# Optimization experiments

Measured on AMD Instinct MI355X. Metric: run time of the kernel, lower is better.

The kernel has to match this reference:

```python
import jax, jax.numpy as jnp
import numpy as np

N_NODES = 200000
N_FRAGS = 50000
N_EDGES = 400000
HDIM = 128
VOCAB = 800


def setup_inputs() -> dict:
    key = jax.random.key(0)
    ks = jax.random.split(key, 9)
    x = jax.random.normal(ks[0], (N_NODES, HDIM), dtype=jnp.float32)
    fragments = jax.random.uniform(ks[1], (N_FRAGS, VOCAB), dtype=jnp.float32)
    emb_table = jax.random.normal(ks[2], (VOCAB, HDIM), dtype=jnp.float32)
    W_f = jax.random.normal(ks[3], (HDIM, HDIM), dtype=jnp.float32) / np.sqrt(HDIM)
    b_f = jax.random.normal(ks[4], (HDIM,), dtype=jnp.float32) * 0.01
    W_s = jax.random.normal(ks[5], (2 * HDIM, HDIM), dtype=jnp.float32) / np.sqrt(2 * HDIM)
    b_s = jax.random.normal(ks[6], (HDIM,), dtype=jnp.float32) * 0.01
    row = jax.random.randint(ks[7], (N_EDGES,), 0, N_NODES, dtype=jnp.int32)
    col = jax.random.randint(ks[8], (N_EDGES,), 0, N_FRAGS, dtype=jnp.int32)
    return {"x": x, "fragments": fragments, "emb_table": emb_table,
            "W_f": W_f, "b_f": b_f, "W_s": W_s, "b_s": b_s,
            "row": row, "col": col}


def _scatter_mean(vals, idx, num_segments):
    s = jax.ops.segment_sum(vals, idx, num_segments=num_segments)
    cnt = jax.ops.segment_sum(jnp.ones((vals.shape[0], 1), vals.dtype), idx,
                              num_segments=num_segments)
    return s / jnp.maximum(cnt, 1.0)


def reference(x, fragments, emb_table, W_f, b_f, W_s, b_s, row, col):
    N, H = x.shape
    F = fragments.shape[0]
    # gather node feats along memberships, mean-pool per fragment: [F, H]
    substructure_x = _scatter_mean(x[row], col, F)
    # fragment type embedding branch
    frag_ids = jnp.argmax(fragments, axis=1)            # [F]
    fragments_emb = emb_table[frag_ids] @ W_f + b_f      # [F, H]
    substructure_x = jnp.concatenate([substructure_x, fragments_emb], axis=1)  # [F, 2H]
    fragment_emb = substructure_x @ W_s + b_s            # [F, H]
    # gather fragment embeddings back to memberships, mean-pool per node: [N, H]
    return _scatter_mean(fragment_emb[col], row, N)
```

## Files before the change

### kernel.cpp

```cpp
#include <hip/hip_runtime.h>

#define HDIM 128
#define VOCAB 800
#define FB 32
#define NB 64
#define TILE 1024
#define TILE_N 512

typedef float f4 __attribute__((ext_vector_type(4)));
typedef float f2 __attribute__((ext_vector_type(2)));

#define ACC8(pa, pb, h) { \
    pa.x += __uint_as_float(h.x << 16); \
    pa.y += __uint_as_float(h.x & 0xffff0000u); \
    pa.z += __uint_as_float(h.y << 16); \
    pa.w += __uint_as_float(h.y & 0xffff0000u); \
    pb.x += __uint_as_float(h.z << 16); \
    pb.y += __uint_as_float(h.z & 0xffff0000u); \
    pb.z += __uint_as_float(h.w << 16); \
    pb.w += __uint_as_float(h.w & 0xffff0000u); }

static __device__ __forceinline__ unsigned short f2bf(float f) {
    unsigned int u = __float_as_uint(f);
    return (unsigned short)((u + 0x7fffu + ((u >> 16) & 1u)) >> 16);
}

__global__ void k_amc(const float* __restrict__ frags, int* __restrict__ frag_id,
                      const float* __restrict__ x, unsigned short* __restrict__ xb,
                      const int* __restrict__ row, const int* __restrict__ col,
                      int* __restrict__ cnt,
                      const float* __restrict__ emb, const float* __restrict__ W_f,
                      const float* __restrict__ W_s, const float* __restrict__ b_f,
                      const float* __restrict__ b_s, float* __restrict__ E2,
                      float* __restrict__ bfs, int F) {
    __shared__ float e[2][HDIM], t1[2][HDIM];
    int b = blockIdx.x, t = threadIdx.x;
    if (b < 12500) {
        int wave = b * 4 + (t >> 6);
        int lane = t & 63;
        const f4* r = reinterpret_cast<const f4*>(frags + (size_t)wave * VOCAB);
        float best = -1e30f;
        int bidx = 0;
        for (int i = lane; i < VOCAB / 4; i += 64) {
            f4 v = __builtin_nontemporal_load(r + i);
            int base = i * 4;
            if (v.x > best) { best = v.x; bidx = base + 0; }
            if (v.y > best) { best = v.y; bidx = base + 1; }
            if (v.z > best) { best = v.z; bidx = base + 2; }
            if (v.w > best) { best = v.w; bidx = base + 3; }
        }
        for (int off = 32; off > 0; off >>= 1) {
            float ov = __shfl_xor(best, off, 64);
            int   oi = __shfl_xor(bidx, off, 64);
            if (ov > best || (ov == best && oi < bidx)) { best = ov; bidx = oi; }
        }
        if (lane == 0) frag_id[wave] = bidx;
    } else if (b < 12891) {
        int i = (b - 12500) * 256 + t;
        if (i < 100000) {
            int4 r4 = reinterpret_cast<const int4*>(row)[i];
            int4 c4 = reinterpret_cast<const int4*>(col)[i];
            atomicAdd(&cnt[F + r4.x], 1); atomicAdd(&cnt[F + r4.y], 1);
            atomicAdd(&cnt[F + r4.z], 1); atomicAdd(&cnt[F + r4.w], 1);
            atomicAdd(&cnt[c4.x], 1); atomicAdd(&cnt[c4.y], 1);
            atomicAdd(&cnt[c4.z], 1); atomicAdd(&cnt[c4.w], 1);
        }
    } else if (b < 25391) {
        size_t i = (size_t)(b - 12891) * 256 + t;
        const f4* xp = reinterpret_cast<const f4*>(x);
        f4 v0 = __builtin_nontemporal_load(xp + 2 * i);
        f4 v1 = __builtin_nontemporal_load(xp + 2 * i + 1);
        uint4 o;
        o.x = (unsigned)f2bf(v0.x) | ((unsigned)f2bf(v0.y) << 16);
        o.y = (unsigned)f2bf(v0.z) | ((unsigned)f2bf(v0.w) << 16);
        o.z = (unsigned)f2bf(v1.x) | ((unsigned)f2bf(v1.y) << 16);
        o.w = (unsigned)f2bf(v1.z) | ((unsigned)f2bf(v1.w) << 16);
        *reinterpret_cast<uint4*>(xb + i * 8) = o;
    } else {
        int bp = b - 25391;
        int j = t & 127, half = t >> 7;
        if (bp < 400) {
            int v = bp * 2 + half;
            e[half][j] = emb[(size_t)v * HDIM + j];
            __syncthreads();
            float a = 0.f;
            for (int k = 0; k < HDIM; ++k)
                a = fmaf(e[half][k], W_f[k * HDIM + j], a);
            t1[half][j] = a;
            __syncthreads();
            float bb = 0.f;
            for (int k = 0; k < HDIM; ++k)
                bb = fmaf(t1[half][k], W_s[(HDIM + k) * HDIM + j], bb);
            E2[(size_t)v * HDIM + j] = bb;
        } else {
            if (half == 0) e[0][j] = b_f[j];
            __syncthreads();
            if (half == 0) {
                float bb = b_s[j];
                for (int k = 0; k < HDIM; ++k)
                    bb = fmaf(e[0][k], W_s[(HDIM + k) * HDIM + j], bb);
                bfs[j] = bb;
            }
        }
    }
}

__global__ void k_bsum(const int* __restrict__ cnt, int L, int* __restrict__ bsum) {
    __shared__ int s[256];
    int t = threadIdx.x;
    int i = blockIdx.x * 256 + t;
    s[t] = (i < L) ? cnt[i] : 0;
    __syncthreads();
    for (int o = 128; o > 0; o >>= 1) {
        if (t < o) s[t] += s[t + o];
        __syncthreads();
    }
    if (t == 0) bsum[blockIdx.x] = s[0];
}

__global__ void k_scan(int* __restrict__ bsum, int nb) {
    __shared__ int s[1024];
    int t = threadIdx.x;
    int v = (t < nb) ? bsum[t] : 0;
    s[t] = v;
    __syncthreads();
    for (int o = 1; o < 1024; o <<= 1) {
        int a = (t >= o) ? s[t - o] : 0;
        __syncthreads();
        s[t] += a;
        __syncthreads();
    }
    if (t < nb) bsum[t] = s[t] - v;
}

__global__ void k_base(const int* __restrict__ cnt, const int* __restrict__ bsum, int L,
                       int* __restrict__ base) {
    __shared__ int s[256];
    int t = threadIdx.x;
    int i = blockIdx.x * 256 + t;
    int v = (i < L) ? cnt[i] : 0;
    s[t] = v;
    __syncthreads();
    for (int o = 1; o < 256; o <<= 1) {
        int a = (t >= o) ? s[t - o] : 0;
        __syncthreads();
        s[t] += a;
        __syncthreads();
    }
    if (i < L) base[i] = bsum[blockIdx.x] + s[t] - v;
}

__global__ void k_place(const int* __restrict__ row, const int* __restrict__ col,
                        int* __restrict__ base, int* __restrict__ pay, int F, int E) {
    int i = blockIdx.x * 256 + threadIdx.x;
    if (i >= E / 4) return;
    int4 r4 = reinterpret_cast<const int4*>(row)[i];
    int4 c4 = reinterpret_cast<const int4*>(col)[i];
#define PL(r, c) { \
    int pc = atomicAdd(&base[c], 1); pay[pc] = r; \
    int pr = atomicAdd(&base[F + r], 1); pay[pr] = c; }
    PL(r4.x, c4.x) PL(r4.y, c4.y) PL(r4.z, c4.z) PL(r4.w, c4.w)
#undef PL
}

__global__ __launch_bounds__(256) void k_frag(
        const unsigned short* __restrict__ xb, const int* __restrict__ base,
        const int* __restrict__ pay, const int* __restrict__ frag_id,
        const float* __restrict__ W_s, const float* __restrict__ E2,
        const float* __restrict__ bfs, unsigned short* __restrict__ fembb, int F, int E) {
    __shared__ f2 sI[FB / 2][HDIM];
    __shared__ int eidx[TILE];
    __shared__ int cb[FB + 1];
    int t = threadIdx.x;
    int sg = t >> 4, l = t & 15;
    int fb = blockIdx.x * FB;
    if (t <= FB) {
        int idx = fb + t - 1;
        cb[t] = (idx < 0) ? 0 : ((idx < F) ? base[idx] : E);
    }
    __syncthreads();
    int st0 = cb[sg],      d0 = cb[sg + 1] - st0;
    int st1 = cb[16 + sg], d1 = cb[17 + sg] - st1;
    int p0 = cb[0], pend = cb[FB];
    const uint4* x4 = reinterpret_cast<const uint4*>(xb);
    float4 z = make_float4(0.f, 0.f, 0.f, 0.f);
    float4 a0A0 = z, a0A1 = z, a0B0 = z, a0B1 = z;
    float4 a1A0 = z, a1A1 = z, a1B0 = z, a1B1 = z;
    for (int tb = p0; tb < pend; tb += TILE) {
        int nload = min(TILE, pend - tb);
        for (int i = t; i < nload; i += 256) eidx[i] = pay[tb + i];
        __syncthreads();
        int lim = tb + nload;
        int lo0 = max(st0, tb) - tb, hi0 = min(st0 + d0, lim) - tb;
        int lo1 = max(st1, tb) - tb, hi1 = min(st1 + d1, lim) - tb;
        int m = max(hi0 - lo0, hi1 - lo1);
        for (int j = 0; j < m; j += 2) {
            if (lo0 + j < hi0)     { uint4 h = x4[(size_t)eidx[lo0 + j]     * 16 + l]; ACC8(a0A0, a0A1, h); }
            if (lo0 + j + 1 < hi0) { uint4 h = x4[(size_t)eidx[lo0 + j + 1] * 16 + l]; ACC8(a0B0, a0B1, h); }
            if (lo1 + j < hi1)     { uint4 h = x4[(size_t)eidx[lo1 + j]     * 16 + l]; ACC8(a1A0, a1A1, h); }
            if (lo1 + j + 1 < hi1) { uint4 h = x4[(size_t)eidx[lo1 + j + 1] * 16 + l]; ACC8(a1B0, a1B1, h); }
        }
        __syncthreads();
    }
    {
        float inv0 = 1.0f / fmaxf((float)d0, 1.0f);
        float inv1 = 1.0f / fmaxf((float)d1, 1.0f);
        int pr0 = sg >> 1, pa0 = sg & 1;
        int pr1 = (16 + sg) >> 1, pa1 = sg & 1;
        float v0[8] = { (a0A0.x + a0B0.x) * inv0, (a0A0.y + a0B0.y) * inv0,
                        (a0A0.z + a0B0.z) * inv0, (a0A0.w + a0B0.w) * inv0,
                        (a0A1.x + a0B1.x) * inv0, (a0A1.y + a0B1.y) * inv0,
                        (a0A1.z + a0B1.z) * inv0, (a0A1.w + a0B1.w) * inv0 };
        float v1[8] = { (a1A0.x + a1B0.x) * inv1, (a1A0.y + a1B0.y) * inv1,
                        (a1A0.z + a1B0.z) * inv1, (a1A0.w + a1B0.w) * inv1,
                        (a1A1.x + a1B1.x) * inv1, (a1A1.y + a1B1.y) * inv1,
                        (a1A1.z + a1B1.z) * inv1, (a1A1.w + a1B1.w) * inv1 };
#pragma unroll
        for (int i = 0; i < 8; ++i) {
            ((float*)&sI[pr0][8 * l + i])[pa0] = v0[i];
            ((float*)&sI[pr1][8 * l + i])[pa1] = v1[i];
        }
    }
    __syncthreads();
    int d = t & 127;
    int fh = t >> 7;
    float bv = bfs[d];
    f2 acc2[8];
#pragma unroll
    for (int q = 0; q < 8; ++q) {
        int pr = fh * 8 + q;
        int fA = fb + 2 * pr, fB = fA + 1;
        int idA = frag_id[min(fA, F - 1)];
        int idB = frag_id[min(fB, F - 1)];
        acc2[q].x = E2[(size_t)idA * HDIM + d] + bv;
        acc2[q].y = E2[(size_t)idB * HDIM + d] + bv;
    }
    for (int k = 0; k < HDIM; k += 2) {
        float w0 = W_s[(k + 0) * HDIM + d];
        float w1 = W_s[(k + 1) * HDIM + d];
        f2 w0v; w0v.x = w0; w0v.y = w0;
        f2 w1v; w1v.x = w1; w1v.y = w1;
#pragma unroll
        for (int q = 0; q < 8; ++q) {
            int pr = fh * 8 + q;
            f2 vv0 = sI[pr][k];
            f2 vv1 = sI[pr][k + 1];
            acc2[q] += vv0 * w0v + vv1 * w1v;
        }
    }
#pragma unroll
    for (int q = 0; q < 8; ++q) {
        int pr = fh * 8 + q;
        int fA = fb + 2 * pr;
        if (fA < F)     fembb[(size_t)fA * HDIM + d]       = f2bf(acc2[q].x);
        if (fA + 1 < F) fembb[(size_t)(fA + 1) * HDIM + d] = f2bf(acc2[q].y);
    }
}

__global__ __launch_bounds__(256) void k_node(
        const unsigned short* __restrict__ fembb, const int* __restrict__ base,
        const int* __restrict__ pay, float* __restrict__ out, int F, int E, int N) {
    __shared__ int eidx[TILE_N];
    __shared__ int cb[NB + 1];
    int t = threadIdx.x;
    int sg = t >> 4, l = t & 15;
    int n0 = blockIdx.x * NB;
    if (t <= NB) {
        int idx = n0 + t - 1;
        cb[t] = (idx < 0) ? E : base[F + idx];
    }
    __syncthreads();
    int st_[4], dg_[4];
    float4 z = make_float4(0.f, 0.f, 0.f, 0.f);
    float4 aA0[4] = {z, z, z, z}, aA1[4] = {z, z, z, z};
    float4 aB0[4] = {z, z, z, z}, aB1[4] = {z, z, z, z};
#pragma unroll
    for (int q = 0; q < 4; ++q) {
        st_[q] = cb[sg * 4 + q];
        dg_[q] = cb[sg * 4 + q + 1] - st_[q];
    }
    int p0 = cb[0], pend = cb[NB];
    const uint4* f4p = reinterpret_cast<const uint4*>(fembb);
    for (int tb = p0; tb < pend; tb += TILE_N) {
        int nload = min(TILE_N, pend - tb);
        for (int i = t; i < nload; i += 256) eidx[i] = pay[tb + i];
        __syncthreads();
        int lim = tb + nload;
        int lo[4], hi[4];
        int m = 0;
#pragma unroll
        for (int q = 0; q < 4; ++q) {
            lo[q] = max(st_[q], tb) - tb;
            hi[q] = min(st_[q] + dg_[q], lim) - tb;
            m = max(m, hi[q] - lo[q]);
        }
        for (int j = 0; j < m; j += 2) {
#pragma unroll
            for (int q = 0; q < 4; ++q) {
                if (lo[q] + j < hi[q])     { uint4 h = f4p[(size_t)eidx[lo[q] + j]     * 16 + l]; ACC8(aA0[q], aA1[q], h); }
                if (lo[q] + j + 1 < hi[q]) { uint4 h = f4p[(size_t)eidx[lo[q] + j + 1] * 16 + l]; ACC8(aB0[q], aB1[q], h); }
            }
        }
        __syncthreads();
    }
    f4* o4 = reinterpret_cast<f4*>(out);
#pragma unroll
    for (int q = 0; q < 4; ++q) {
        float inv = 1.0f / fmaxf((float)dg_[q], 1.0f);
        f4 w0, w1;
        w0.x = (aA0[q].x + aB0[q].x) * inv; w0.y = (aA0[q].y + aB0[q].y) * inv;
        w0.z = (aA0[q].z + aB0[q].z) * inv; w0.w = (aA0[q].w + aB0[q].w) * inv;
        w1.x = (aA1[q].x + aB1[q].x) * inv; w1.y = (aA1[q].y + aB1[q].y) * inv;
        w1.z = (aA1[q].z + aB1[q].z) * inv; w1.w = (aA1[q].w + aB1[q].w) * inv;
        size_t nrow = (size_t)(n0 + sg * 4 + q) * 32;
        __builtin_nontemporal_store(w0, o4 + nrow + 2 * l + 0);
        __builtin_nontemporal_store(w1, o4 + nrow + 2 * l + 1);
    }
}

extern "C" void kernel_launch(void* const* d_in, const int* in_sizes, int n_in,
                              void* d_out, int out_size, void* d_ws, size_t ws_size,
                              hipStream_t stream) {
    const float* x         = (const float*)d_in[0];
    const float* fragments = (const float*)d_in[1];
    const float* emb_table = (const float*)d_in[2];
    const float* W_f       = (const float*)d_in[3];
    const float* b_f       = (const float*)d_in[4];
    const float* W_s       = (const float*)d_in[5];
    const float* b_s       = (const float*)d_in[6];
    const int*   row       = (const int*)d_in[7];
    const int*   col       = (const int*)d_in[8];
    float* out = (float*)d_out;

    const int N = 200000, F = 50000, E = 400000;
    const int L = F + N;
    const int NBT = (L + 255) / 256;

    unsigned short* xb = (unsigned short*)d_out;

    unsigned short* fembb = (unsigned short*)d_ws;
    int* cnt     = (int*)(fembb + (size_t)F * HDIM);
    int* base    = cnt + L;
    int* bsum    = base + L;
    int* pay     = bsum + 1024;
    int* frag_id = pay + 2 * E;
    float* E2    = (float*)(frag_id + F);
    float* bfs   = E2 + VOCAB * HDIM;

    hipMemsetAsync(cnt, 0, (size_t)L * sizeof(int), stream);

    k_amc<<<25792, 256, 0, stream>>>(fragments, frag_id, x, xb, row, col, cnt,
                                     emb_table, W_f, W_s, b_f, b_s, E2, bfs, F);
    k_bsum<<<NBT, 256, 0, stream>>>(cnt, L, bsum);
    k_scan<<<1, 1024, 0, stream>>>(bsum, NBT);
    k_base<<<NBT, 256, 0, stream>>>(cnt, bsum, L, base);
    k_place<<<(E / 4 + 255) / 256, 256, 0, stream>>>(row, col, base, pay, F, E);
    k_frag<<<(F + FB - 1) / FB, 256, 0, stream>>>(xb, base, pay, frag_id, W_s, E2, bfs,
                                                  fembb, F, E);
    k_node<<<N / NB, 256, 0, stream>>>(fembb, base, pay, out, F, E, N);
}
```

Before: 241.8 us.

## Counting-sort fragments and nodes by degree to balance gather work

```diff
diff --git a/kernel.cpp b/kernel.cpp
--- a/kernel.cpp
+++ b/kernel.cpp
@@ -105,79 +105,114 @@
     }
 }
 
-__global__ void k_bsum(const int* __restrict__ cnt, int L, int* __restrict__ bsum) {
-    __shared__ int s[256];
+__global__ void k_hist(const int* __restrict__ cnt, int* __restrict__ hist, int F, int N) {
+    __shared__ int lh[512];
     int t = threadIdx.x;
+    lh[t] = 0; lh[256 + t] = 0;
+    __syncthreads();
     int i = blockIdx.x * 256 + t;
-    s[t] = (i < L) ? cnt[i] : 0;
-    __syncthreads();
-    for (int o = 128; o > 0; o >>= 1) {
-        if (t < o) s[t] += s[t + o];
-        __syncthreads();
-    }
-    if (t == 0) bsum[blockIdx.x] = s[0];
-}
-
-__global__ void k_scan(int* __restrict__ bsum, int nb) {
-    __shared__ int s[1024];
+    if (i < F + N) {
+        int d = min(cnt[i], 255);
+        atomicAdd(&lh[(i < F ? 0 : 256) + d], 1);
+    }
+    __syncthreads();
+    if (lh[t]) atomicAdd(&hist[t], lh[t]);
+    if (lh[256 + t]) atomicAdd(&hist[256 + t], lh[256 + t]);
+}
+
+__global__ void k_scan256(const int* __restrict__ hist, int* __restrict__ bstart,
+                          int* __restrict__ bedge, int* __restrict__ gslotcur,
+                          int* __restrict__ bs_c, int* __restrict__ bs_r,
+                          int F, int N, int E) {
+    __shared__ int s1[256], s2[256];
+    int tb = blockIdx.x * 256;
     int t = threadIdx.x;
-    int v = (t < nb) ? bsum[t] : 0;
-    s[t] = v;
-    __syncthreads();
-    for (int o = 1; o < 1024; o <<= 1) {
-        int a = (t >= o) ? s[t - o] : 0;
-        __syncthreads();
-        s[t] += a;
-        __syncthreads();
-    }
-    if (t < nb) bsum[t] = s[t] - v;
-}
-
-__global__ void k_base(const int* __restrict__ cnt, const int* __restrict__ bsum, int L,
-                       int* __restrict__ base) {
-    __shared__ int s[256];
+    int h = hist[tb + t];
+    int v1 = h, v2 = h * t;
+    s1[t] = v1; s2[t] = v2;
+    __syncthreads();
+    for (int o = 1; o < 256; o <<= 1) {
+        int a1 = (t >= o) ? s1[t - o] : 0;
+        int a2 = (t >= o) ? s2[t - o] : 0;
+        __syncthreads();
+        s1[t] += a1; s2[t] += a2;
+        __syncthreads();
+    }
+    bstart[tb + t] = s1[t] - v1;
+    bedge[tb + t]  = s2[t] - v2;
+    gslotcur[tb + t] = s1[t] - v1;
+    if (t == 0) {
+        if (blockIdx.x == 0) bs_c[F] = E;
+        else                 bs_r[N] = 2 * E;
+    }
+}
+
+__global__ void k_slot(const int* __restrict__ cnt, const int* __restrict__ bstart,
+                       const int* __restrict__ bedge, int* __restrict__ gslotcur,
+                       int* __restrict__ islot, int* __restrict__ permc,
+                       int* __restrict__ permr, int* __restrict__ bs_c,
+                       int* __restrict__ bs_r, int* __restrict__ cur,
+                       int F, int N, int E, int NBC) {
+    __shared__ int lh[256], lbase[256];
     int t = threadIdx.x;
-    int i = blockIdx.x * 256 + t;
-    int v = (i < L) ? cnt[i] : 0;
-    s[t] = v;
-    __syncthreads();
-    for (int o = 1; o < 256; o <<= 1) {
-        int a = (t >= o) ? s[t - o] : 0;
-        __syncthreads();
-        s[t] += a;
-        __syncthreads();
-    }
-    if (i < L) base[i] = bsum[blockIdx.x] + s[t] - v;
+    bool isFrag = (int)blockIdx.x < NBC;
+    int tb = isFrag ? 0 : 256;
+    int i = (isFrag ? blockIdx.x : (blockIdx.x - NBC)) * 256 + t;
+    int L = isFrag ? F : N;
+    int d = (i < L) ? cnt[(isFrag ? 0 : F) + i] : -1;
+    int b = (d >= 0) ? min(d, 255) : -1;
+    lh[t] = 0;
+    __syncthreads();
+    int r = (b >= 0) ? atomicAdd(&lh[b], 1) : 0;
+    __syncthreads();
+    if (lh[t] > 0) lbase[t] = atomicAdd(&gslotcur[tb + t], lh[t]);
+    __syncthreads();
+    if (b >= 0) {
+        int sp = lbase[b] + r;
+        int eo = bedge[tb + b] + (sp - bstart[tb + b]) * b;
+        if (isFrag) {
+            islot[i] = sp;
+            permc[sp] = i;
+            bs_c[sp] = eo;
+            cur[sp] = eo;
+        } else {
+            islot[F + i] = sp;
+            permr[sp] = i;
+            bs_r[sp] = E + eo;
+            cur[F + sp] = E + eo;
+        }
+    }
 }
 
 __global__ void k_place(const int* __restrict__ row, const int* __restrict__ col,
-                        int* __restrict__ base, int* __restrict__ pay, int F, int E) {
+                        const int* __restrict__ islot, int* __restrict__ cur,
+                        int* __restrict__ pay, int F, int E) {
     int i = blockIdx.x * 256 + threadIdx.x;
     if (i >= E / 4) return;
     int4 r4 = reinterpret_cast<const int4*>(row)[i];
     int4 c4 = reinterpret_cast<const int4*>(col)[i];
 #define PL(r, c) { \
-    int pc = atomicAdd(&base[c], 1); pay[pc] = r; \
-    int pr = atomicAdd(&base[F + r], 1); pay[pr] = c; }
+    int sc = islot[c]; int pc = atomicAdd(&cur[sc], 1); pay[pc] = r; \
+    int sr = islot[F + r]; int pr = atomicAdd(&cur[F + sr], 1); pay[pr] = c; }
     PL(r4.x, c4.x) PL(r4.y, c4.y) PL(r4.z, c4.z) PL(r4.w, c4.w)
 #undef PL
 }
 
 __global__ __launch_bounds__(256) void k_frag(
-        const unsigned short* __restrict__ xb, const int* __restrict__ base,
-        const int* __restrict__ pay, const int* __restrict__ frag_id,
-        const float* __restrict__ W_s, const float* __restrict__ E2,
-        const float* __restrict__ bfs, unsigned short* __restrict__ fembb, int F, int E) {
+        const unsigned short* __restrict__ xb, const int* __restrict__ bs_c,
+        const int* __restrict__ pay, const int* __restrict__ permc,
+        const int* __restrict__ frag_id, const float* __restrict__ W_s,
+        const float* __restrict__ E2, const float* __restrict__ bfs,
+        unsigned short* __restrict__ fembb, int F, int E) {
     __shared__ f2 sI[FB / 2][HDIM];
     __shared__ int eidx[TILE];
     __shared__ int cb[FB + 1];
+    __shared__ int pm[FB];
     int t = threadIdx.x;
     int sg = t >> 4, l = t & 15;
-    int fb = blockIdx.x * FB;
-    if (t <= FB) {
-        int idx = fb + t - 1;
-        cb[t] = (idx < 0) ? 0 : ((idx < F) ? base[idx] : E);
-    }
+    int sb = blockIdx.x * FB;
+    if (t <= FB) cb[t] = bs_c[min(sb + t, F)];
+    if (t < FB)  pm[t] = (sb + t < F) ? permc[sb + t] : 0;
     __syncthreads();
     int st0 = cb[sg],      d0 = cb[sg + 1] - st0;
     int st1 = cb[16 + sg], d1 = cb[17 + sg] - st1;
@@ -229,11 +264,9 @@
 #pragma unroll
     for (int q = 0; q < 8; ++q) {
         int pr = fh * 8 + q;
-        int fA = fb + 2 * pr, fB = fA + 1;
-        int idA = frag_id[min(fA, F - 1)];
-        int idB = frag_id[min(fB, F - 1)];
-        acc2[q].x = E2[(size_t)idA * HDIM + d] + bv;
-        acc2[q].y = E2[(size_t)idB * HDIM + d] + bv;
+        int oA = pm[2 * pr], oB = pm[2 * pr + 1];
+        acc2[q].x = E2[(size_t)frag_id[oA] * HDIM + d] + bv;
+        acc2[q].y = E2[(size_t)frag_id[oB] * HDIM + d] + bv;
     }
     for (int k = 0; k < HDIM; k += 2) {
         float w0 = W_s[(k + 0) * HDIM + d];
@@ -251,24 +284,24 @@
 #pragma unroll
     for (int q = 0; q < 8; ++q) {
         int pr = fh * 8 + q;
-        int fA = fb + 2 * pr;
-        if (fA < F)     fembb[(size_t)fA * HDIM + d]       = f2bf(acc2[q].x);
-        if (fA + 1 < F) fembb[(size_t)(fA + 1) * HDIM + d] = f2bf(acc2[q].y);
+        int slotA = sb + 2 * pr;
+        if (slotA < F)     fembb[(size_t)pm[2 * pr]     * HDIM + d] = f2bf(acc2[q].x);
+        if (slotA + 1 < F) fembb[(size_t)pm[2 * pr + 1] * HDIM + d] = f2bf(acc2[q].y);
     }
 }
 
 __global__ __launch_bounds__(256) void k_node(
-        const unsigned short* __restrict__ fembb, const int* __restrict__ base,
-        const int* __restrict__ pay, float* __restrict__ out, int F, int E, int N) {
+        const unsigned short* __restrict__ fembb, const int* __restrict__ bs_r,
+        const int* __restrict__ pay, const int* __restrict__ permr,
+        float* __restrict__ out, int N) {
     __shared__ int eidx[TILE_N];
     __shared__ int cb[NB + 1];
+    __shared__ int pm[NB];
     int t = threadIdx.x;
     int sg = t >> 4, l = t & 15;
     int n0 = blockIdx.x * NB;
-    if (t <= NB) {
-        int idx = n0 + t - 1;
-        cb[t] = (idx < 0) ? E : base[F + idx];
-    }
+    if (t <= NB) cb[t] = bs_r[min(n0 + t, N)];
+    if (t < NB)  pm[t] = permr[n0 + t];
     __syncthreads();
     int st_[4], dg_[4];
     float4 z = make_float4(0.f, 0.f, 0.f, 0.f);
@@ -312,7 +345,7 @@
         w0.z = (aA0[q].z + aB0[q].z) * inv; w0.w = (aA0[q].w + aB0[q].w) * inv;
         w1.x = (aA1[q].x + aB1[q].x) * inv; w1.y = (aA1[q].y + aB1[q].y) * inv;
         w1.z = (aA1[q].z + aB1[q].z) * inv; w1.w = (aA1[q].w + aB1[q].w) * inv;
-        size_t nrow = (size_t)(n0 + sg * 4 + q) * 32;
+        size_t nrow = (size_t)pm[sg * 4 + q] * 32;
         __builtin_nontemporal_store(w0, o4 + nrow + 2 * l + 0);
         __builtin_nontemporal_store(w1, o4 + nrow + 2 * l + 1);
     }
@@ -334,28 +367,38 @@
 
     const int N = 200000, F = 50000, E = 400000;
     const int L = F + N;
-    const int NBT = (L + 255) / 256;
+    const int NBC = (F + 255) / 256;
+    const int NBR = (N + 255) / 256;
 
     unsigned short* xb = (unsigned short*)d_out;
 
     unsigned short* fembb = (unsigned short*)d_ws;
-    int* cnt     = (int*)(fembb + (size_t)F * HDIM);
-    int* base    = cnt + L;
-    int* bsum    = base + L;
-    int* pay     = bsum + 1024;
-    int* frag_id = pay + 2 * E;
-    float* E2    = (float*)(frag_id + F);
-    float* bfs   = E2 + VOCAB * HDIM;
-
-    hipMemsetAsync(cnt, 0, (size_t)L * sizeof(int), stream);
+    int* cnt      = (int*)(fembb + (size_t)F * HDIM);
+    int* hist     = cnt + L;
+    int* bstart   = hist + 512;
+    int* bedge    = bstart + 512;
+    int* gslotcur = bedge + 512;
+    int* islot    = gslotcur + 512;
+    int* permc    = islot + L;
+    int* permr    = permc + F;
+    int* bs_c     = permr + N;
+    int* bs_r     = bs_c + F + 1;
+    int* cur      = bs_r + N + 1;
+    int* pay      = cur + L;
+    int* frag_id  = pay + 2 * E;
+    float* E2     = (float*)(frag_id + F);
+    float* bfs    = E2 + VOCAB * HDIM;
+
+    hipMemsetAsync(cnt, 0, (size_t)(L + 512) * sizeof(int), stream);
 
     k_amc<<<25792, 256, 0, stream>>>(fragments, frag_id, x, xb, row, col, cnt,
                                      emb_table, W_f, W_s, b_f, b_s, E2, bfs, F);
-    k_bsum<<<NBT, 256, 0, stream>>>(cnt, L, bsum);
-    k_scan<<<1, 1024, 0, stream>>>(bsum, NBT);
-    k_base<<<NBT, 256, 0, stream>>>(cnt, bsum, L, base);
-    k_place<<<(E / 4 + 255) / 256, 256, 0, stream>>>(row, col, base, pay, F, E);
-    k_frag<<<(F + FB - 1) / FB, 256, 0, stream>>>(xb, base, pay, frag_id, W_s, E2, bfs,
-                                                  fembb, F, E);
-    k_node<<<N / NB, 256, 0, stream>>>(fembb, base, pay, out, F, E, N);
-}
+    k_hist<<<(L + 255) / 256, 256, 0, stream>>>(cnt, hist, F, N);
+    k_scan256<<<2, 256, 0, stream>>>(hist, bstart, bedge, gslotcur, bs_c, bs_r, F, N, E);
+    k_slot<<<NBC + NBR, 256, 0, stream>>>(cnt, bstart, bedge, gslotcur, islot,
+                                          permc, permr, bs_c, bs_r, cur, F, N, E, NBC);
+    k_place<<<(E / 4 + 255) / 256, 256, 0, stream>>>(row, col, islot, cur, pay, F, E);
+    k_frag<<<(F + FB - 1) / FB, 256, 0, stream>>>(xb, bs_c, pay, permc, frag_id,
+                                                  W_s, E2, bfs, fembb, F, E);
+    k_node<<<N / NB, 256, 0, stream>>>(fembb, bs_r, pay, permr, out, N);
+}
```

Result: slower. 262.1 us (+8.4%).
